# Optimization experiments

Hardware: AMD Instinct MI355X
Metric: run time of the kernel (lower is better)

Reference implementation:

```python
import jax, jax.numpy as jnp
import numpy as np

S, N, H, O = 128, 2048, 128, 128  # seq_len(=input_size), num_samples, hidden_size, output_size


def setup_inputs() -> dict:
    key = jax.random.key(0)
    ks = jax.random.split(key, 7)
    scale = 1.0 / np.sqrt(H)
    u = lambda k, shp: jax.random.uniform(k, shp, jnp.float32, -scale, scale)
    return {
        "x": jax.random.normal(ks[0], (S, N, H), jnp.float32),
        "W_ih": u(ks[1], (4 * H, H)),   # PyTorch gate order: i, f, g, o
        "W_hh": u(ks[2], (4 * H, H)),
        "b_ih": u(ks[3], (4 * H,)),
        "b_hh": u(ks[4], (4 * H,)),
        "W_out": u(ks[5], (O, H)),
        "b_out": u(ks[6], (O,)),
    }


def _lstm_forward(x, W_ih, W_hh, b_ih, b_hh, W_out, b_out):
    n, h = x.shape[1], W_hh.shape[1]
    # Precompute input contribution to gates for all timesteps: [S, N, 4H]
    xg = jnp.einsum("snh,gh->sng", x, W_ih) + (b_ih + b_hh)

    def step(carry, xt):
        h_t, c_t = carry
        gates = xt + h_t @ W_hh.T  # [N, 4H]
        i, f, g, o = jnp.split(gates, 4, axis=-1)
        i = jax.nn.sigmoid(i)
        f = jax.nn.sigmoid(f)
        g = jnp.tanh(g)
        o = jax.nn.sigmoid(o)
        c_t = f * c_t + i * g
        h_t = o * jnp.tanh(c_t)
        return (h_t, c_t), h_t

    h0 = jnp.zeros((n, h), x.dtype)  # init_hidden(): zeros
    c0 = jnp.zeros((n, h), x.dtype)
    _, out = jax.lax.scan(step, (h0, c0), xg)  # out: [S, N, H]
    # Linear projection fused over all timesteps
    pred = jnp.einsum("snh,oh->sno", out, W_out) + b_out  # [S, N, O]
    return pred


def reference(x, W_ih, W_hh, b_ih, b_hh, W_out, b_out):
    return _lstm_forward(x, W_ih, W_hh, b_ih, b_hh, W_out, b_out)
```

## Files before the change

kernel.cpp:

```cpp
#include <hip/hip_runtime.h>
#include <hip/hip_bf16.h>


#define S_LEN   128
#define N_BATCH 2048
#define H_DIM   128
#define O_DIM   128

using short8  = __attribute__((ext_vector_type(8))) short;
using short4v = __attribute__((ext_vector_type(4))) short;
using floatx4 = __attribute__((ext_vector_type(4))) float;
typedef unsigned short u16;

#define ROWP     264
#define BUFELEMS (16 * ROWP)

__device__ __forceinline__ u16 f2b(float f) {
    unsigned int u = __float_as_uint(f);
    return (u16)((u + 0x7FFF + ((u >> 16) & 1)) >> 16);
}
__device__ __forceinline__ short8 pack8s(const float* p, float k) {
    short8 r;
#pragma unroll
    for (int i = 0; i < 8; ++i) r[i] = (short)f2b(k * p[i]);
    return r;
}
__device__ __forceinline__ short4v pack4(float4 f) {
    short4v r;
    r[0] = (short)f2b(f.x); r[1] = (short)f2b(f.y);
    r[2] = (short)f2b(f.z); r[3] = (short)f2b(f.w);
    return r;
}
__device__ __forceinline__ float tanhf_fast(float v) {
    return 1.0f - 2.0f * __builtin_amdgcn_rcpf(1.0f + __builtin_amdgcn_exp2f(2.8853900817779268f * v));
}

__device__ __forceinline__ void lds_barrier() {
    asm volatile("s_waitcnt lgkmcnt(0)" ::: "memory");
    __builtin_amdgcn_s_barrier();
}

__device__ __forceinline__ void step_body(
    int s,
    floatx4& g0, floatx4& g1, floatx4& g2, floatx4& g3,
    floatx4& n0v, floatx4& n1v, floatx4& n2v, floatx4& n3v,
    const short* shb, short* shn, short* stagep,
    const short8 (&wh)[4][4], const short8 (&wx)[4][4], const short8 (&wo)[4],
    const float (&biasv)[4], float bo,
    float (&cc)[4], float4& xcur, const float*& xptr, float*& pcur,
    int arow, int hcol, int qrow)
{
    floatx4 ao = {bo, bo, bo, bo};

#pragma unroll
    for (int kk = 0; kk < 4; ++kk) {
        short8 ah = *reinterpret_cast<const short8*>(&shb[arow + 128 + kk * 32]);
        g0 = __builtin_amdgcn_mfma_f32_16x16x32_bf16(ah, wh[0][kk], g0, 0, 0, 0);
        g1 = __builtin_amdgcn_mfma_f32_16x16x32_bf16(ah, wh[1][kk], g1, 0, 0, 0);
        g2 = __builtin_amdgcn_mfma_f32_16x16x32_bf16(ah, wh[2][kk], g2, 0, 0, 0);
        g3 = __builtin_amdgcn_mfma_f32_16x16x32_bf16(ah, wh[3][kk], g3, 0, 0, 0);
        ao = __builtin_amdgcn_mfma_f32_16x16x32_bf16(ah, wo[kk], ao, 0, 0, 0);
    }

    if (s > 0) {
#pragma unroll
        for (int r = 0; r < 4; ++r)
            pcur[(size_t)r * O_DIM] = ao[r];
        pcur += (size_t)N_BATCH * O_DIM;
    }

    if (s < S_LEN - 1) {
        n0v = floatx4{biasv[0], biasv[0], biasv[0], biasv[0]};
        n1v = floatx4{biasv[1], biasv[1], biasv[1], biasv[1]};
        n2v = floatx4{biasv[2], biasv[2], biasv[2], biasv[2]};
        n3v = floatx4{biasv[3], biasv[3], biasv[3], biasv[3]};
#pragma unroll
        for (int kk = 0; kk < 4; ++kk) {
            short8 axv = *reinterpret_cast<const short8*>(&shb[arow + kk * 32]);
            n0v = __builtin_amdgcn_mfma_f32_16x16x32_bf16(axv, wx[0][kk], n0v, 0, 0, 0);
            n1v = __builtin_amdgcn_mfma_f32_16x16x32_bf16(axv, wx[1][kk], n1v, 0, 0, 0);
            n2v = __builtin_amdgcn_mfma_f32_16x16x32_bf16(axv, wx[2][kk], n2v, 0, 0, 0);
            n3v = __builtin_amdgcn_mfma_f32_16x16x32_bf16(axv, wx[3][kk], n3v, 0, 0, 0);
        }
    }

    if (s <= S_LEN - 3)
        *reinterpret_cast<short4v*>(stagep) = pack4(xcur);
    if (s <= S_LEN - 4)
        xcur = *reinterpret_cast<const float4*>(xptr);
    xptr += (size_t)N_BATCH * H_DIM;

#pragma unroll
    for (int r = 0; r < 4; ++r) {
        float iv = __builtin_amdgcn_rcpf(1.0f + __builtin_amdgcn_exp2f(g0[r]));
        float fv = __builtin_amdgcn_rcpf(1.0f + __builtin_amdgcn_exp2f(g1[r]));
        float gv = 1.0f - 2.0f * __builtin_amdgcn_rcpf(1.0f + __builtin_amdgcn_exp2f(g2[r]));
        float ov = __builtin_amdgcn_rcpf(1.0f + __builtin_amdgcn_exp2f(g3[r]));
        cc[r] = fv * cc[r] + iv * gv;
        shn[(qrow + r) * ROWP + hcol] = (short)f2b(ov * tanhf_fast(cc[r]));
    }

    lds_barrier();
}

__global__ __launch_bounds__(512, 2)
void lstm_persist(const float* __restrict__ x,
                  const float* __restrict__ W_ih,
                  const float* __restrict__ W_hh,
                  const float* __restrict__ b_ih,
                  const float* __restrict__ b_hh,
                  const float* __restrict__ W_out,
                  const float* __restrict__ b_out,
                  float* __restrict__ pred) {
    __shared__ short sh[2 * BUFELEMS];

    const int tid  = (int)threadIdx.x;
    const int wave = tid >> 6;
    const int lane = tid & 63;
    const int quad = lane >> 4;
    const int l15  = lane & 15;
    const int n0   = (int)blockIdx.x * 16;

    const float kSig = -1.4426950408889634f;
    const float kG   =  2.8853900817779268f;

    short8 wx[4][4], wh[4][4], wo[4];
    float  biasv[4];
#pragma unroll
    for (int t = 0; t < 4; ++t) {
        const float sc = (t == 2) ? kG : kSig;
        const int g = t * 128 + wave * 16 + l15;
#pragma unroll
        for (int kk = 0; kk < 4; ++kk) {
            wx[t][kk] = pack8s(W_ih + g * H_DIM + kk * 32 + quad * 8, sc);
            wh[t][kk] = pack8s(W_hh + g * H_DIM + kk * 32 + quad * 8, sc);
        }
        biasv[t] = sc * (b_ih[g] + b_hh[g]);
    }
    const int ocol = wave * 16 + l15;
#pragma unroll
    for (int kk = 0; kk < 4; ++kk)
        wo[kk] = pack8s(W_out + ocol * H_DIM + kk * 32 + quad * 8, 1.0f);
    const float bo = b_out[ocol];

    const int xm = tid >> 5;
    const int xq = (tid & 31) * 4;

    for (int i = tid; i < 16 * 128; i += 512)
        sh[(i >> 7) * ROWP + 128 + (i & 127)] = 0;
    {
        float4 f0 = *reinterpret_cast<const float4*>(x + ((size_t)(n0 + xm)) * H_DIM + xq);
        float4 f1 = *reinterpret_cast<const float4*>(x + ((size_t)N_BATCH + n0 + xm) * H_DIM + xq);
        *reinterpret_cast<short4v*>(&sh[BUFELEMS + xm * ROWP + xq]) = pack4(f0);
        *reinterpret_cast<short4v*>(&sh[xm * ROWP + xq]) = pack4(f1);
    }
    float4 xcur = *reinterpret_cast<const float4*>(x + ((size_t)2 * N_BATCH + n0 + xm) * H_DIM + xq);
    __syncthreads();

    const int arow = l15 * ROWP + quad * 8;
    const int hcol = 128 + wave * 16 + l15;
    const int qrow = quad * 4;

    floatx4 xgA0 = {biasv[0], biasv[0], biasv[0], biasv[0]};
    floatx4 xgA1 = {biasv[1], biasv[1], biasv[1], biasv[1]};
    floatx4 xgA2 = {biasv[2], biasv[2], biasv[2], biasv[2]};
    floatx4 xgA3 = {biasv[3], biasv[3], biasv[3], biasv[3]};
#pragma unroll
    for (int kk = 0; kk < 4; ++kk) {
        short8 a = *reinterpret_cast<const short8*>(&sh[BUFELEMS + arow + kk * 32]);
        xgA0 = __builtin_amdgcn_mfma_f32_16x16x32_bf16(a, wx[0][kk], xgA0, 0, 0, 0);
        xgA1 = __builtin_amdgcn_mfma_f32_16x16x32_bf16(a, wx[1][kk], xgA1, 0, 0, 0);
        xgA2 = __builtin_amdgcn_mfma_f32_16x16x32_bf16(a, wx[2][kk], xgA2, 0, 0, 0);
        xgA3 = __builtin_amdgcn_mfma_f32_16x16x32_bf16(a, wx[3][kk], xgA3, 0, 0, 0);
    }
    __syncthreads();

    floatx4 xgB0, xgB1, xgB2, xgB3;
    float cc[4] = {0.f, 0.f, 0.f, 0.f};

    short* const sA = sh;
    short* const sB = sh + BUFELEMS;
    short* const stageA = &sA[xm * ROWP + xq];
    short* const stageB = &sB[xm * ROWP + xq];

    const float* xptr = x + (size_t)3 * N_BATCH * H_DIM + ((size_t)(n0 + xm)) * H_DIM + xq;
    float*       pcur = pred + ((size_t)(n0 + qrow)) * O_DIM + wave * 16 + l15;

    for (int it = 0; it < S_LEN / 2; ++it) {
        step_body(2 * it,     xgA0, xgA1, xgA2, xgA3, xgB0, xgB1, xgB2, xgB3,
                  sA, sB, stageB, wh, wx, wo, biasv, bo, cc, xcur, xptr, pcur,
                  arow, hcol, qrow);
        step_body(2 * it + 1, xgB0, xgB1, xgB2, xgB3, xgA0, xgA1, xgA2, xgA3,
                  sB, sA, stageA, wh, wx, wo, biasv, bo, cc, xcur, xptr, pcur,
                  arow, hcol, qrow);
    }

    floatx4 ao = {bo, bo, bo, bo};
#pragma unroll
    for (int kk = 0; kk < 4; ++kk) {
        short8 ah = *reinterpret_cast<const short8*>(&sh[arow + 128 + kk * 32]);
        ao = __builtin_amdgcn_mfma_f32_16x16x32_bf16(ah, wo[kk], ao, 0, 0, 0);
    }
#pragma unroll
    for (int r = 0; r < 4; ++r)
        pcur[(size_t)r * O_DIM] = ao[r];
}

extern "C" void kernel_launch(void* const* d_in, const int* in_sizes, int n_in,
                              void* d_out, int out_size, void* d_ws, size_t ws_size,
                              hipStream_t stream) {
    const float* x    = (const float*)d_in[0];
    const float* Wih  = (const float*)d_in[1];
    const float* Whh  = (const float*)d_in[2];
    const float* bih  = (const float*)d_in[3];
    const float* bhh  = (const float*)d_in[4];
    const float* Wout = (const float*)d_in[5];
    const float* bout = (const float*)d_in[6];
    float* pred = (float*)d_out;

    lstm_persist<<<dim3(N_BATCH / 16), dim3(512), 0, stream>>>(
        x, Wih, Whh, bih, bhh, Wout, bout, pred);
}
```

Before: 344.9 us.

## Split batch into 8-row blocks of four waves covering 32 gate columns each

Launches twice as many blocks, each with half the threads, handling 8 batch rows instead of 16. Each wave now owns two 16-column gate tiles, so per-wave weight registers and MFMA count double. The aim is to fill all CUs with the persistent recurrent loop and give each wave more independent MFMAs between barriers. In exchange, half of each 16-row MFMA tile is spent on duplicated rows, and register pressure rises sharply, which could cause spilling.

Result: slower. 454.2 us (+31.7%).

```diff
diff --git a/kernel.cpp b/kernel.cpp
--- a/kernel.cpp
+++ b/kernel.cpp
@@ -42,68 +42,85 @@
 
 __device__ __forceinline__ void step_body(
     int s,
-    floatx4& g0, floatx4& g1, floatx4& g2, floatx4& g3,
-    floatx4& n0v, floatx4& n1v, floatx4& n2v, floatx4& n3v,
+    floatx4 (&g)[4][2], floatx4 (&n)[4][2],
     const short* shb, short* shn, short* stagep,
-    const short8 (&wh)[4][4], const short8 (&wx)[4][4], const short8 (&wo)[4],
-    const float (&biasv)[4], float bo,
-    float (&cc)[4], float4& xcur, const float*& xptr, float*& pcur,
-    int arow, int hcol, int qrow)
+    const short8 (&wh)[4][4][2], const short8 (&wx)[4][4][2],
+    const short8 (&wo)[4][2],
+    const float (&biasv)[4][2], const float (&bo)[2],
+    float (&cc)[2][4], float4& xc0, float4& xc1,
+    const float*& xptr, float*& pcur,
+    int arow, int hcolb, int qrow, bool predrow)
 {
-    floatx4 ao = {bo, bo, bo, bo};
+    floatx4 ao[2];
+#pragma unroll
+    for (int cf = 0; cf < 2; ++cf)
+        ao[cf] = floatx4{bo[cf], bo[cf], bo[cf], bo[cf]};
 
 #pragma unroll
     for (int kk = 0; kk < 4; ++kk) {
         short8 ah = *reinterpret_cast<const short8*>(&shb[arow + 128 + kk * 32]);
-        g0 = __builtin_amdgcn_mfma_f32_16x16x32_bf16(ah, wh[0][kk], g0, 0, 0, 0);
-        g1 = __builtin_amdgcn_mfma_f32_16x16x32_bf16(ah, wh[1][kk], g1, 0, 0, 0);
-        g2 = __builtin_amdgcn_mfma_f32_16x16x32_bf16(ah, wh[2][kk], g2, 0, 0, 0);
-        g3 = __builtin_amdgcn_mfma_f32_16x16x32_bf16(ah, wh[3][kk], g3, 0, 0, 0);
-        ao = __builtin_amdgcn_mfma_f32_16x16x32_bf16(ah, wo[kk], ao, 0, 0, 0);
-    }
-
-    if (s > 0) {
-#pragma unroll
-        for (int r = 0; r < 4; ++r)
-            pcur[(size_t)r * O_DIM] = ao[r];
-        pcur += (size_t)N_BATCH * O_DIM;
-    }
+#pragma unroll
+        for (int t = 0; t < 4; ++t) {
+            g[t][0] = __builtin_amdgcn_mfma_f32_16x16x32_bf16(ah, wh[t][kk][0], g[t][0], 0, 0, 0);
+            g[t][1] = __builtin_amdgcn_mfma_f32_16x16x32_bf16(ah, wh[t][kk][1], g[t][1], 0, 0, 0);
+        }
+        ao[0] = __builtin_amdgcn_mfma_f32_16x16x32_bf16(ah, wo[kk][0], ao[0], 0, 0, 0);
+        ao[1] = __builtin_amdgcn_mfma_f32_16x16x32_bf16(ah, wo[kk][1], ao[1], 0, 0, 0);
+    }
+
+    if (s > 0 && predrow) {
+#pragma unroll
+        for (int cf = 0; cf < 2; ++cf)
+#pragma unroll
+            for (int r = 0; r < 4; ++r)
+                pcur[(size_t)r * O_DIM + cf * 16] = ao[cf][r];
+    }
+    if (s > 0) pcur += (size_t)N_BATCH * O_DIM;
 
     if (s < S_LEN - 1) {
-        n0v = floatx4{biasv[0], biasv[0], biasv[0], biasv[0]};
-        n1v = floatx4{biasv[1], biasv[1], biasv[1], biasv[1]};
-        n2v = floatx4{biasv[2], biasv[2], biasv[2], biasv[2]};
-        n3v = floatx4{biasv[3], biasv[3], biasv[3], biasv[3]};
+#pragma unroll
+        for (int t = 0; t < 4; ++t) {
+            n[t][0] = floatx4{biasv[t][0], biasv[t][0], biasv[t][0], biasv[t][0]};
+            n[t][1] = floatx4{biasv[t][1], biasv[t][1], biasv[t][1], biasv[t][1]};
+        }
 #pragma unroll
         for (int kk = 0; kk < 4; ++kk) {
             short8 axv = *reinterpret_cast<const short8*>(&shb[arow + kk * 32]);
-            n0v = __builtin_amdgcn_mfma_f32_16x16x32_bf16(axv, wx[0][kk], n0v, 0, 0, 0);
-            n1v = __builtin_amdgcn_mfma_f32_16x16x32_bf16(axv, wx[1][kk], n1v, 0, 0, 0);
-            n2v = __builtin_amdgcn_mfma_f32_16x16x32_bf16(axv, wx[2][kk], n2v, 0, 0, 0);
-            n3v = __builtin_amdgcn_mfma_f32_16x16x32_bf16(axv, wx[3][kk], n3v, 0, 0, 0);
-        }
-    }
-
-    if (s <= S_LEN - 3)
-        *reinterpret_cast<short4v*>(stagep) = pack4(xcur);
-    if (s <= S_LEN - 4)
-        xcur = *reinterpret_cast<const float4*>(xptr);
+#pragma unroll
+            for (int t = 0; t < 4; ++t) {
+                n[t][0] = __builtin_amdgcn_mfma_f32_16x16x32_bf16(axv, wx[t][kk][0], n[t][0], 0, 0, 0);
+                n[t][1] = __builtin_amdgcn_mfma_f32_16x16x32_bf16(axv, wx[t][kk][1], n[t][1], 0, 0, 0);
+            }
+        }
+    }
+
+    if (s <= S_LEN - 3) {
+        *reinterpret_cast<short4v*>(stagep)     = pack4(xc0);
+        *reinterpret_cast<short4v*>(stagep + 4) = pack4(xc1);
+    }
+    if (s <= S_LEN - 4) {
+        xc0 = *reinterpret_cast<const float4*>(xptr);
+        xc1 = *reinterpret_cast<const float4*>(xptr + 4);
+    }
     xptr += (size_t)N_BATCH * H_DIM;
 
 #pragma unroll
-    for (int r = 0; r < 4; ++r) {
-        float iv = __builtin_amdgcn_rcpf(1.0f + __builtin_amdgcn_exp2f(g0[r]));
-        float fv = __builtin_amdgcn_rcpf(1.0f + __builtin_amdgcn_exp2f(g1[r]));
-        float gv = 1.0f - 2.0f * __builtin_amdgcn_rcpf(1.0f + __builtin_amdgcn_exp2f(g2[r]));
-        float ov = __builtin_amdgcn_rcpf(1.0f + __builtin_amdgcn_exp2f(g3[r]));
-        cc[r] = fv * cc[r] + iv * gv;
-        shn[(qrow + r) * ROWP + hcol] = (short)f2b(ov * tanhf_fast(cc[r]));
+    for (int cf = 0; cf < 2; ++cf) {
+#pragma unroll
+        for (int r = 0; r < 4; ++r) {
+            float iv = __builtin_amdgcn_rcpf(1.0f + __builtin_amdgcn_exp2f(g[0][cf][r]));
+            float fv = __builtin_amdgcn_rcpf(1.0f + __builtin_amdgcn_exp2f(g[1][cf][r]));
+            float gv = 1.0f - 2.0f * __builtin_amdgcn_rcpf(1.0f + __builtin_amdgcn_exp2f(g[2][cf][r]));
+            float ov = __builtin_amdgcn_rcpf(1.0f + __builtin_amdgcn_exp2f(g[3][cf][r]));
+            cc[cf][r] = fv * cc[cf][r] + iv * gv;
+            shn[(qrow + r) * ROWP + hcolb + cf * 16] = (short)f2b(ov * tanhf_fast(cc[cf][r]));
+        }
     }
 
     lds_barrier();
 }
 
-__global__ __launch_bounds__(512, 2)
+__global__ __launch_bounds__(256, 1)
 void lstm_persist(const float* __restrict__ x,
                   const float* __restrict__ W_ih,
                   const float* __restrict__ W_hh,
@@ -119,91 +136,110 @@
     const int lane = tid & 63;
     const int quad = lane >> 4;
     const int l15  = lane & 15;
-    const int n0   = (int)blockIdx.x * 16;
+    const int n0   = (int)blockIdx.x * 8;
 
     const float kSig = -1.4426950408889634f;
     const float kG   =  2.8853900817779268f;
 
-    short8 wx[4][4], wh[4][4], wo[4];
-    float  biasv[4];
+    short8 wx[4][4][2], wh[4][4][2], wo[4][2];
+    float  biasv[4][2], bo[2];
 #pragma unroll
     for (int t = 0; t < 4; ++t) {
         const float sc = (t == 2) ? kG : kSig;
-        const int g = t * 128 + wave * 16 + l15;
-#pragma unroll
-        for (int kk = 0; kk < 4; ++kk) {
-            wx[t][kk] = pack8s(W_ih + g * H_DIM + kk * 32 + quad * 8, sc);
-            wh[t][kk] = pack8s(W_hh + g * H_DIM + kk * 32 + quad * 8, sc);
-        }
-        biasv[t] = sc * (b_ih[g] + b_hh[g]);
-    }
-    const int ocol = wave * 16 + l15;
-#pragma unroll
-    for (int kk = 0; kk < 4; ++kk)
-        wo[kk] = pack8s(W_out + ocol * H_DIM + kk * 32 + quad * 8, 1.0f);
-    const float bo = b_out[ocol];
-
-    const int xm = tid >> 5;
-    const int xq = (tid & 31) * 4;
-
-    for (int i = tid; i < 16 * 128; i += 512)
+#pragma unroll
+        for (int cf = 0; cf < 2; ++cf) {
+            const int g = t * 128 + wave * 32 + cf * 16 + l15;
+#pragma unroll
+            for (int kk = 0; kk < 4; ++kk) {
+                wx[t][kk][cf] = pack8s(W_ih + g * H_DIM + kk * 32 + quad * 8, sc);
+                wh[t][kk][cf] = pack8s(W_hh + g * H_DIM + kk * 32 + quad * 8, sc);
+            }
+            biasv[t][cf] = sc * (b_ih[g] + b_hh[g]);
+        }
+    }
+#pragma unroll
+    for (int cf = 0; cf < 2; ++cf) {
+        const int ocol = wave * 32 + cf * 16 + l15;
+#pragma unroll
+        for (int kk = 0; kk < 4; ++kk)
+            wo[kk][cf] = pack8s(W_out + ocol * H_DIM + kk * 32 + quad * 8, 1.0f);
+        bo[cf] = b_out[ocol];
+    }
+
+    const int xm  = tid >> 4;
+    const int xq  = (tid & 15) * 8;
+    const int xgr = n0 + (xm & 7);
+
+    for (int i = tid; i < 16 * 128; i += 256)
         sh[(i >> 7) * ROWP + 128 + (i & 127)] = 0;
     {
-        float4 f0 = *reinterpret_cast<const float4*>(x + ((size_t)(n0 + xm)) * H_DIM + xq);
-        float4 f1 = *reinterpret_cast<const float4*>(x + ((size_t)N_BATCH + n0 + xm) * H_DIM + xq);
-        *reinterpret_cast<short4v*>(&sh[BUFELEMS + xm * ROWP + xq]) = pack4(f0);
-        *reinterpret_cast<short4v*>(&sh[xm * ROWP + xq]) = pack4(f1);
-    }
-    float4 xcur = *reinterpret_cast<const float4*>(x + ((size_t)2 * N_BATCH + n0 + xm) * H_DIM + xq);
+        const float* r0 = x + (size_t)xgr * H_DIM + xq;
+        const float* r1 = x + ((size_t)N_BATCH + xgr) * H_DIM + xq;
+        *reinterpret_cast<short4v*>(&sh[BUFELEMS + xm * ROWP + xq])     = pack4(*reinterpret_cast<const float4*>(r0));
+        *reinterpret_cast<short4v*>(&sh[BUFELEMS + xm * ROWP + xq + 4]) = pack4(*reinterpret_cast<const float4*>(r0 + 4));
+        *reinterpret_cast<short4v*>(&sh[xm * ROWP + xq])     = pack4(*reinterpret_cast<const float4*>(r1));
+        *reinterpret_cast<short4v*>(&sh[xm * ROWP + xq + 4]) = pack4(*reinterpret_cast<const float4*>(r1 + 4));
+    }
+    float4 xc0 = *reinterpret_cast<const float4*>(x + ((size_t)2 * N_BATCH + xgr) * H_DIM + xq);
+    float4 xc1 = *reinterpret_cast<const float4*>(x + ((size_t)2 * N_BATCH + xgr) * H_DIM + xq + 4);
     __syncthreads();
 
-    const int arow = l15 * ROWP + quad * 8;
-    const int hcol = 128 + wave * 16 + l15;
-    const int qrow = quad * 4;
-
-    floatx4 xgA0 = {biasv[0], biasv[0], biasv[0], biasv[0]};
-    floatx4 xgA1 = {biasv[1], biasv[1], biasv[1], biasv[1]};
-    floatx4 xgA2 = {biasv[2], biasv[2], biasv[2], biasv[2]};
-    floatx4 xgA3 = {biasv[3], biasv[3], biasv[3], biasv[3]};
+    const int arow  = l15 * ROWP + quad * 8;
+    const int hcolb = 128 + wave * 32 + l15;
+    const int qrow  = quad * 4;
+    const bool predrow = (quad < 2);
+
+    floatx4 xgA[4][2], xgB[4][2];
+#pragma unroll
+    for (int t = 0; t < 4; ++t) {
+        xgA[t][0] = floatx4{biasv[t][0], biasv[t][0], biasv[t][0], biasv[t][0]};
+        xgA[t][1] = floatx4{biasv[t][1], biasv[t][1], biasv[t][1], biasv[t][1]};
+    }
 #pragma unroll
     for (int kk = 0; kk < 4; ++kk) {
         short8 a = *reinterpret_cast<const short8*>(&sh[BUFELEMS + arow + kk * 32]);
-        xgA0 = __builtin_amdgcn_mfma_f32_16x16x32_bf16(a, wx[0][kk], xgA0, 0, 0, 0);
-        xgA1 = __builtin_amdgcn_mfma_f32_16x16x32_bf16(a, wx[1][kk], xgA1, 0, 0, 0);
-        xgA2 = __builtin_amdgcn_mfma_f32_16x16x32_bf16(a, wx[2][kk], xgA2, 0, 0, 0);
-        xgA3 = __builtin_amdgcn_mfma_f32_16x16x32_bf16(a, wx[3][kk], xgA3, 0, 0, 0);
+#pragma unroll
+        for (int t = 0; t < 4; ++t) {
+            xgA[t][0] = __builtin_amdgcn_mfma_f32_16x16x32_bf16(a, wx[t][kk][0], xgA[t][0], 0, 0, 0);
+            xgA[t][1] = __builtin_amdgcn_mfma_f32_16x16x32_bf16(a, wx[t][kk][1], xgA[t][1], 0, 0, 0);
+        }
     }
     __syncthreads();
 
-    floatx4 xgB0, xgB1, xgB2, xgB3;
-    float cc[4] = {0.f, 0.f, 0.f, 0.f};
+    float cc[2][4] = {{0.f,0.f,0.f,0.f},{0.f,0.f,0.f,0.f}};
 
     short* const sA = sh;
     short* const sB = sh + BUFELEMS;
     short* const stageA = &sA[xm * ROWP + xq];
     short* const stageB = &sB[xm * ROWP + xq];
 
-    const float* xptr = x + (size_t)3 * N_BATCH * H_DIM + ((size_t)(n0 + xm)) * H_DIM + xq;
-    float*       pcur = pred + ((size_t)(n0 + qrow)) * O_DIM + wave * 16 + l15;
+    const float* xptr = x + ((size_t)3 * N_BATCH + xgr) * H_DIM + xq;
+    float*       pcur = pred + ((size_t)(n0 + qrow)) * O_DIM + wave * 32 + l15;
 
     for (int it = 0; it < S_LEN / 2; ++it) {
-        step_body(2 * it,     xgA0, xgA1, xgA2, xgA3, xgB0, xgB1, xgB2, xgB3,
-                  sA, sB, stageB, wh, wx, wo, biasv, bo, cc, xcur, xptr, pcur,
-                  arow, hcol, qrow);
-        step_body(2 * it + 1, xgB0, xgB1, xgB2, xgB3, xgA0, xgA1, xgA2, xgA3,
-                  sB, sA, stageA, wh, wx, wo, biasv, bo, cc, xcur, xptr, pcur,
-                  arow, hcol, qrow);
-    }
-
-    floatx4 ao = {bo, bo, bo, bo};
+        step_body(2 * it,     xgA, xgB, sA, sB, stageB, wh, wx, wo, biasv, bo,
+                  cc, xc0, xc1, xptr, pcur, arow, hcolb, qrow, predrow);
+        step_body(2 * it + 1, xgB, xgA, sB, sA, stageA, wh, wx, wo, biasv, bo,
+                  cc, xc0, xc1, xptr, pcur, arow, hcolb, qrow, predrow);
+    }
+
+    floatx4 ao[2];
+#pragma unroll
+    for (int cf = 0; cf < 2; ++cf)
+        ao[cf] = floatx4{bo[cf], bo[cf], bo[cf], bo[cf]};
 #pragma unroll
     for (int kk = 0; kk < 4; ++kk) {
         short8 ah = *reinterpret_cast<const short8*>(&sh[arow + 128 + kk * 32]);
-        ao = __builtin_amdgcn_mfma_f32_16x16x32_bf16(ah, wo[kk], ao, 0, 0, 0);
-    }
-#pragma unroll
-    for (int r = 0; r < 4; ++r)
-        pcur[(size_t)r * O_DIM] = ao[r];
+        ao[0] = __builtin_amdgcn_mfma_f32_16x16x32_bf16(ah, wo[kk][0], ao[0], 0, 0, 0);
+        ao[1] = __builtin_amdgcn_mfma_f32_16x16x32_bf16(ah, wo[kk][1], ao[1], 0, 0, 0);
+    }
+    if (predrow) {
+#pragma unroll
+        for (int cf = 0; cf < 2; ++cf)
+#pragma unroll
+            for (int r = 0; r < 4; ++r)
+                pcur[(size_t)r * O_DIM + cf * 16] = ao[cf][r];
+    }
 }
 
 extern "C" void kernel_launch(void* const* d_in, const int* in_sizes, int n_in,
@@ -218,6 +254,6 @@
     const float* bout = (const float*)d_in[6];
     float* pred = (float*)d_out;
 
-    lstm_persist<<<dim3(N_BATCH / 16), dim3(512), 0, stream>>>(
+    lstm_persist<<<dim3(N_BATCH / 8), dim3(256), 0, stream>>>(
         x, Wih, Whh, bih, bhh, Wout, bout, pred);
 }
```
